# Optimization experiments

Hardware: AMD Instinct MI355X
Metric: run time of the kernel (lower is better)

The kernel has to match this reference:

```python
import jax, jax.numpy as jnp
import numpy as np

N = 50000      # nodes
E = 640000     # edges
D = 128        # emb_dim
IN_DIM = 64    # raw node feature dim
L = 5          # num_layer
BN_EPS = 1e-5


def setup_inputs() -> dict:
    key = jax.random.key(0)
    ks = jax.random.split(key, 12)
    s = 0.05  # modest init scale
    return {
        "x": jax.random.normal(ks[0], (N, IN_DIM), jnp.float32),
        "edge_index": jax.random.randint(ks[1], (2, E), 0, N, jnp.int32),
        "edge_attr": jax.random.normal(ks[2], (E, 13), jnp.float32),
        "atom_W": jax.random.normal(ks[3], (IN_DIM, D), jnp.float32) * s,
        "atom_b": jnp.zeros((D,), jnp.float32),
        "bond_W": jax.random.normal(ks[4], (L, 13, D), jnp.float32) * s,
        "bond_b": jnp.zeros((L, D), jnp.float32),
        "W1": jax.random.normal(ks[5], (L, D, 2 * D), jnp.float32) * s,
        "b1": jnp.zeros((L, 2 * D), jnp.float32),
        "bn1_g": jnp.ones((L, 2 * D), jnp.float32),
        "bn1_b": jnp.zeros((L, 2 * D), jnp.float32),
        "W2": jax.random.normal(ks[6], (L, 2 * D, D), jnp.float32) * s,
        "b2": jnp.zeros((L, D), jnp.float32),
        "eps": jnp.zeros((L,), jnp.float32),
        "bn_g": jnp.ones((L, D), jnp.float32),
        "bn_b": jnp.zeros((L, D), jnp.float32),
    }


def _batchnorm(h, g, b):
    # training-mode BatchNorm1d: batch stats over node axis, biased variance
    mu = jnp.mean(h, axis=0)
    var = jnp.mean(jnp.square(h - mu), axis=0)
    return g * (h - mu) * jax.lax.rsqrt(var + BN_EPS) + b


def reference(x, edge_index, edge_attr, atom_W, atom_b, bond_W, bond_b,
              W1, b1, bn1_g, bn1_b, W2, b2, eps, bn_g, bn_b):
    src, dst = edge_index[0], edge_index[1]
    n = x.shape[0]
    h = x @ atom_W + atom_b  # atom_encoder, [N, D]
    for l in range(L):
        # GINConv: gather -> add edge embedding -> relu -> scatter-add
        edge_emb = edge_attr @ bond_W[l] + bond_b[l]              # [E, D]
        msg = jax.nn.relu(h[src] + edge_emb)                      # [E, D]
        agg = jax.ops.segment_sum(msg, dst, num_segments=n)       # [N, D]
        z = (1.0 + eps[l]) * h + agg
        # mlp: Linear -> BN -> ReLU -> Linear
        z = _batchnorm(z @ W1[l] + b1[l], bn1_g[l], bn1_b[l])
        z = jax.nn.relu(z)
        z = z @ W2[l] + b2[l]
        # outer batchnorm; relu on all but last layer (dropout is eval no-op)
        z = _batchnorm(z, bn_g[l], bn_b[l])
        if l < L - 1:
            z = jax.nn.relu(z)
        h = z  # residual=False, JK='last'
    return h
```

## Files before the change

kernel.cpp:

```cpp
#include <hip/hip_runtime.h>
#include <stdint.h>

#define N_NODES 50000
#define N_EDGES 640000
#define DIM 128
#define IN_DIM 64
#define LAYERS 5
#define BN_EPS 1e-5f
#define NBLK 782

typedef __attribute__((ext_vector_type(8))) short short8;
typedef __attribute__((ext_vector_type(4))) float f32x4;

__device__ __forceinline__ unsigned short f32_to_bf16(float f) {
    uint32_t u = __float_as_uint(f);
    u += 0x7fffu + ((u >> 16) & 1u);
    return (unsigned short)(u >> 16);
}
__device__ __forceinline__ float bf16_to_f32(unsigned short h) {
    return __uint_as_float(((uint32_t)h) << 16);
}

__global__ void wtrans(const float* __restrict__ W, unsigned short* __restrict__ WH,
                       unsigned short* __restrict__ WL, int K, int NN, int total) {
    int idx = blockIdx.x * 256 + threadIdx.x;
    if (idx >= total) return;
    int per = K * NN;
    int l = idx / per;
    int r = idx - l * per;
    int k = r / NN;
    int n = r - k * NN;
    float v = W[idx];
    unsigned short hi = f32_to_bf16(v);
    unsigned short lo = f32_to_bf16(v - bf16_to_f32(hi));
    WH[l * per + n * K + k] = hi;
    WL[l * per + n * K + k] = lo;
}

__global__ __launch_bounds__(256) void atom_enc(const float* __restrict__ x,
                                                const float* __restrict__ W,
                                                const float* __restrict__ b,
                                                float* __restrict__ h) {
    __shared__ float Wl[IN_DIM * DIM];
    __shared__ float bl[DIM];
    for (int i = threadIdx.x; i < IN_DIM * DIM; i += 256) Wl[i] = W[i];
    if (threadIdx.x < DIM) bl[threadIdx.x] = b[threadIdx.x];
    __syncthreads();
    int col = threadIdx.x & 127;
    int rh  = threadIdx.x >> 7;
    int row0 = blockIdx.x * 32;
    for (int rr = 0; rr < 16; ++rr) {
        int row = row0 + rr * 2 + rh;
        if (row >= N_NODES) return;
        float acc = bl[col];
        const float* xr = x + row * IN_DIM;
        #pragma unroll
        for (int k = 0; k < IN_DIM; k += 4) {
            float4 xv = *(const float4*)(xr + k);
            acc += xv.x * Wl[(k + 0) * DIM + col];
            acc += xv.y * Wl[(k + 1) * DIM + col];
            acc += xv.z * Wl[(k + 2) * DIM + col];
            acc += xv.w * Wl[(k + 3) * DIM + col];
        }
        h[row * DIM + col] = acc;
    }
}

__global__ void count_deg(const int* __restrict__ ei, int* __restrict__ deg) {
    int e = blockIdx.x * 256 + threadIdx.x;
    if (e < N_EDGES) atomicAdd(&deg[ei[N_EDGES + e]], 1);
}

__global__ __launch_bounds__(1024) void scan_off(const int* __restrict__ deg,
                                                 int* __restrict__ off,
                                                 int* __restrict__ cursor) {
    __shared__ int wsum[16];
    __shared__ int carry_s;
    int tid = threadIdx.x, w = tid >> 6, lane = tid & 63;
    if (tid == 0) carry_s = 0;
    __syncthreads();
    for (int base = 0; base < N_NODES; base += 1024) {
        int i = base + tid;
        int v = (i < N_NODES) ? deg[i] : 0;
        int x = v;
        #pragma unroll
        for (int d = 1; d < 64; d <<= 1) {
            int t = __shfl_up(x, d);
            if (lane >= d) x += t;
        }
        if (lane == 63) wsum[w] = x;
        __syncthreads();
        if (w == 0) {
            int s_ = (lane < 16) ? wsum[lane] : 0;
            #pragma unroll
            for (int d = 1; d < 16; d <<= 1) {
                int t = __shfl_up(s_, d);
                if (lane >= d) s_ += t;
            }
            if (lane < 16) wsum[lane] = s_;
        }
        __syncthreads();
        int wbase = (w == 0) ? 0 : wsum[w - 1];
        int excl = carry_s + wbase + x - v;
        if (i < N_NODES) { off[i] = excl; cursor[i] = excl; }
        int chunk_total = wsum[15];
        __syncthreads();
        if (tid == 0) carry_s += chunk_total;
        __syncthreads();
    }
    if (threadIdx.x == 0) off[N_NODES] = carry_s;
}

__global__ void fill_csr(const int* __restrict__ ei, int* __restrict__ cursor,
                         int* __restrict__ esrc, int* __restrict__ eidx) {
    int e = blockIdx.x * 256 + threadIdx.x;
    if (e >= N_EDGES) return;
    int dst = ei[N_EDGES + e];
    int pos = atomicAdd(&cursor[dst], 1);
    esrc[pos] = ei[e];
    eidx[pos] = e;
}

__global__ __launch_bounds__(256) void agg_csr(const int* __restrict__ off,
                                               const int* __restrict__ esrc,
                                               const int* __restrict__ eidx,
                                               const float* __restrict__ ea,
                                               const float* __restrict__ bW,
                                               const float* __restrict__ bb,
                                               const float* __restrict__ h,
                                               const float* __restrict__ eps,
                                               int l, float* __restrict__ zf) {
    __shared__ float Wl[13 * DIM];
    __shared__ float bl[DIM];
    for (int i = threadIdx.x; i < 13 * DIM; i += 256) Wl[i] = bW[i];
    if (threadIdx.x < DIM) bl[threadIdx.x] = bb[threadIdx.x];
    __syncthreads();
    int w = threadIdx.x >> 6, lane = threadIdx.x & 63;
    int n = blockIdx.x * 4 + w;
    int c0 = lane * 2;
    float w0[13], w1[13];
    #pragma unroll
    for (int k = 0; k < 13; ++k) { w0[k] = Wl[k * DIM + c0]; w1[k] = Wl[k * DIM + c0 + 1]; }
    float b0 = bl[c0], b1v = bl[c0 + 1];
    int e0 = __builtin_amdgcn_readfirstlane(off[n]);
    int e1 = __builtin_amdgcn_readfirstlane(off[n + 1]);
    int deg = e1 - e0;
    int t = e0 + lane;
    int my_src = (t < e1) ? esrc[t] : 0;
    int my_eid = (t < e1) ? eidx[t] : 0;
    int cnt = deg < 64 ? deg : 64;
    float ax = 0.f, ay = 0.f;

    float a_[13]; float2 hv;
    if (cnt > 0) {
        int s_ = __shfl(my_src, 0), e_ = __shfl(my_eid, 0);
        const float* p = ea + (size_t)e_ * 13;
        #pragma unroll
        for (int k = 0; k < 13; ++k) a_[k] = p[k];
        hv = *(const float2*)(h + (size_t)s_ * DIM + c0);
    }
    for (int i = 0; i < cnt; ++i) {
        float nb[13]; float2 nh;
        if (i + 1 < cnt) {
            int s_ = __shfl(my_src, i + 1), e_ = __shfl(my_eid, i + 1);
            const float* p = ea + (size_t)e_ * 13;
            #pragma unroll
            for (int k = 0; k < 13; ++k) nb[k] = p[k];
            nh = *(const float2*)(h + (size_t)s_ * DIM + c0);
        }
        float ex = b0, ey = b1v;
        #pragma unroll
        for (int k = 0; k < 13; ++k) {
            ex = fmaf(a_[k], w0[k], ex);
            ey = fmaf(a_[k], w1[k], ey);
        }
        ax += fmaxf(hv.x + ex, 0.f);
        ay += fmaxf(hv.y + ey, 0.f);
        if (i + 1 < cnt) {
            #pragma unroll
            for (int k = 0; k < 13; ++k) a_[k] = nb[k];
            hv = nh;
        }
    }
    for (int s2 = e0 + 64; s2 < e1; ++s2) {
        int src = __builtin_amdgcn_readfirstlane(esrc[s2]);
        int eid = __builtin_amdgcn_readfirstlane(eidx[s2]);
        const float* p = ea + (size_t)eid * 13;
        float ex = b0, ey = b1v;
        #pragma unroll
        for (int k = 0; k < 13; ++k) {
            float a = p[k];
            ex = fmaf(a, w0[k], ex);
            ey = fmaf(a, w1[k], ey);
        }
        float2 hvv = *(const float2*)(h + (size_t)src * DIM + c0);
        ax += fmaxf(hvv.x + ex, 0.f);
        ay += fmaxf(hvv.y + ey, 0.f);
    }
    float sc = 1.0f + eps[l];
    float2 hn = *(const float2*)(h + (size_t)n * DIM + c0);
    float2 o;
    o.x = fmaf(sc, hn.x, ax);
    o.y = fmaf(sc, hn.y, ay);
    *(float2*)(zf + (size_t)n * DIM + c0) = o;
}

template<int K, int NN, int NC, bool FUSE_BN>
__global__ __launch_bounds__(256) void gemm_split(const float* __restrict__ A,
                                                  const unsigned short* __restrict__ BH,
                                                  const unsigned short* __restrict__ BL,
                                                  const float* __restrict__ bias,
                                                  const float* __restrict__ bn_a,
                                                  const float* __restrict__ bn_b,
                                                  float* __restrict__ C,
                                                  float* __restrict__ Ps,
                                                  float* __restrict__ Pss) {
    constexpr int NFRAG = NC / 16;
    __shared__ float red[4][2][NC];
    int w = threadIdx.x >> 6, lane = threadIdx.x & 63;
    int rt = blockIdx.x * 4 + w;
    int row0 = rt * 16;
    int gy = blockIdx.y;
    bool active = row0 < N_NODES;
    int lrow = lane & 15;
    int lk   = (lane >> 4) * 8;
    f32x4 acc[NFRAG];
    #pragma unroll
    for (int f = 0; f < NFRAG; ++f) acc[f] = (f32x4){0.f, 0.f, 0.f, 0.f};
    if (active) {
        const float* Ap = A + (size_t)(row0 + lrow) * K + lk;
        #pragma unroll
        for (int ks = 0; ks < K / 32; ++ks) {
            float av[8];
            *(float4*)(av)     = *(const float4*)(Ap + ks * 32);
            *(float4*)(av + 4) = *(const float4*)(Ap + ks * 32 + 4);
            if (FUSE_BN) {
                #pragma unroll
                for (int j = 0; j < 8; ++j) {
                    int k = ks * 32 + lk + j;
                    av[j] = fmaxf(fmaf(bn_a[k], av[j], bn_b[k]), 0.f);
                }
            }
            short8 ah, al;
            #pragma unroll
            for (int j = 0; j < 8; ++j) {
                unsigned short hi = f32_to_bf16(av[j]);
                ah[j] = (short)hi;
                al[j] = (short)f32_to_bf16(av[j] - bf16_to_f32(hi));
            }
            #pragma unroll
            for (int f = 0; f < NFRAG; ++f) {
                int gcol = gy * NC + f * 16 + lrow;
                short8 bh  = *(const short8*)(BH + (size_t)gcol * K + ks * 32 + lk);
                short8 blv = *(const short8*)(BL + (size_t)gcol * K + ks * 32 + lk);
                acc[f] = __builtin_amdgcn_mfma_f32_16x16x32_bf16(ah, bh,  acc[f], 0, 0, 0);
                acc[f] = __builtin_amdgcn_mfma_f32_16x16x32_bf16(al, bh,  acc[f], 0, 0, 0);
                acc[f] = __builtin_amdgcn_mfma_f32_16x16x32_bf16(ah, blv, acc[f], 0, 0, 0);
            }
        }
    }
    int rbase = row0 + (lane >> 4) * 4;
    #pragma unroll
    for (int f = 0; f < NFRAG; ++f) {
        float cs = 0.f, css = 0.f;
        if (active) {
            int gcol = gy * NC + f * 16 + lrow;
            float bv = bias[gcol];
            #pragma unroll
            for (int r = 0; r < 4; ++r) {
                float v = acc[f][r] + bv;
                C[(size_t)(rbase + r) * NN + gcol] = v;
                cs += v;
                css += v * v;
            }
            cs += __shfl_xor(cs, 16);  css += __shfl_xor(css, 16);
            cs += __shfl_xor(cs, 32);  css += __shfl_xor(css, 32);
        }
        if (lane < 16) {
            red[w][0][f * 16 + lrow] = cs;
            red[w][1][f * 16 + lrow] = css;
        }
    }
    __syncthreads();
    int tid = threadIdx.x;
    if (tid < NC) {
        float v = red[0][0][tid] + red[1][0][tid] + red[2][0][tid] + red[3][0][tid];
        Ps[((size_t)gy * NBLK + blockIdx.x) * NC + tid] = v;
    } else if (tid < 2 * NC) {
        int c = tid - NC;
        float v = red[0][1][c] + red[1][1][c] + red[2][1][c] + red[3][1][c];
        Pss[((size_t)gy * NBLK + blockIdx.x) * NC + c] = v;
    }
}

__global__ void reduce_bn(const float* __restrict__ Ps, const float* __restrict__ Pss,
                          const float* __restrict__ g, const float* __restrict__ bvec,
                          float* __restrict__ a, float* __restrict__ bias,
                          int NC, int C) {
    int w = threadIdx.x >> 6, lane = threadIdx.x & 63;
    int col = blockIdx.x * 4 + w;
    if (col >= C) return;
    int gy = col / NC, lc = col - gy * NC;
    const float* ps  = Ps  + ((size_t)gy * NBLK) * NC + lc;
    const float* pss = Pss + ((size_t)gy * NBLK) * NC + lc;
    float s = 0.f, ss = 0.f;
    for (int b = lane; b < NBLK; b += 64) {
        s  += ps[(size_t)b * NC];
        ss += pss[(size_t)b * NC];
    }
    #pragma unroll
    for (int d = 1; d < 64; d <<= 1) {
        s += __shfl_xor(s, d);
        ss += __shfl_xor(ss, d);
    }
    if (lane == 0) {
        float mu  = s * (1.0f / N_NODES);
        float var = ss * (1.0f / N_NODES) - mu * mu;
        float inv = rsqrtf(var + BN_EPS);
        float av = g[col] * inv;
        a[col] = av;
        bias[col] = bvec[col] - mu * av;
    }
}

__global__ void bn_apply(const float* __restrict__ z, const float* __restrict__ a,
                         const float* __restrict__ bias, float* __restrict__ o,
                         int total, int nmask, int relu) {
    int i = blockIdx.x * 256 + threadIdx.x;
    int base = i * 4;
    if (base >= total) return;
    int col = base & nmask;
    float4 v = *(const float4*)(z + base);
    float4 r;
    r.x = a[col + 0] * v.x + bias[col + 0];
    r.y = a[col + 1] * v.y + bias[col + 1];
    r.z = a[col + 2] * v.z + bias[col + 2];
    r.w = a[col + 3] * v.w + bias[col + 3];
    if (relu) {
        r.x = fmaxf(r.x, 0.f); r.y = fmaxf(r.y, 0.f);
        r.z = fmaxf(r.z, 0.f); r.w = fmaxf(r.w, 0.f);
    }
    *(float4*)(o + base) = r;
}

extern "C" void kernel_launch(void* const* d_in, const int* in_sizes, int n_in,
                              void* d_out, int out_size, void* d_ws, size_t ws_size,
                              hipStream_t stream) {
    const float* x      = (const float*)d_in[0];
    const int*   ei     = (const int*)d_in[1];
    const float* ea     = (const float*)d_in[2];
    const float* atom_W = (const float*)d_in[3];
    const float* atom_b = (const float*)d_in[4];
    const float* bond_W = (const float*)d_in[5];
    const float* bond_b = (const float*)d_in[6];
    const float* W1     = (const float*)d_in[7];
    const float* b1     = (const float*)d_in[8];
    const float* bn1_g  = (const float*)d_in[9];
    const float* bn1_b  = (const float*)d_in[10];
    const float* W2     = (const float*)d_in[11];
    const float* b2     = (const float*)d_in[12];
    const float* eps    = (const float*)d_in[13];
    const float* bn_g   = (const float*)d_in[14];
    const float* bn_b   = (const float*)d_in[15];
    float* out = (float*)d_out;

    uint8_t* ws = (uint8_t*)d_ws;
    float* h   = (float*)(ws + 0);
    float* zf  = (float*)(ws + 25600000);
    float* y1  = (float*)(ws + 51200000);
    unsigned short* W1H = (unsigned short*)(ws + 102400000);
    unsigned short* W1L = (unsigned short*)(ws + 102727680);
    unsigned short* W2H = (unsigned short*)(ws + 103055360);
    unsigned short* W2L = (unsigned short*)(ws + 103383040);
    float* coef  = (float*)(ws + 103710720);
    int* off     = (int*)(ws + 103714816);
    int* cursor  = (int*)(ws + 103914880);
    int* esrc    = (int*)(ws + 104114944);
    int* eidx    = (int*)(ws + 106674944);
    int* deg     = (int*)(ws + 109234944);
    float* Ps1   = (float*)(ws + 109434944);
    float* Pss1  = (float*)(ws + 110235712);
    float* Ps2   = (float*)(ws + 111036480);
    float* Pss2  = (float*)(ws + 111436864);
    float* a1  = coef;       float* bb1 = a1 + 256;
    float* a2  = bb1 + 256;  float* bb2 = a2 + 128;
    float* z2  = zf;

    wtrans<<<640, 256, 0, stream>>>(W1, W1H, W1L, 128, 256, LAYERS * 128 * 256);
    wtrans<<<640, 256, 0, stream>>>(W2, W2H, W2L, 256, 128, LAYERS * 256 * 128);

    atom_enc<<<1563, 256, 0, stream>>>(x, atom_W, atom_b, h);

    hipMemsetAsync(deg, 0, 200000, stream);
    count_deg<<<2500, 256, 0, stream>>>(ei, deg);
    scan_off<<<1, 1024, 0, stream>>>(deg, off, cursor);
    fill_csr<<<2500, 256, 0, stream>>>(ei, cursor, esrc, eidx);

    for (int l = 0; l < LAYERS; ++l) {
        agg_csr<<<12500, 256, 0, stream>>>(
            off, esrc, eidx, ea, bond_W + l * 13 * DIM, bond_b + l * DIM, h, eps, l, zf);

        gemm_split<128, 256, 64, false><<<dim3(NBLK, 4), 256, 0, stream>>>(
            zf, W1H + l * 256 * 128, W1L + l * 256 * 128, b1 + l * 256,
            nullptr, nullptr, y1, Ps1, Pss1);

        reduce_bn<<<64, 256, 0, stream>>>(Ps1, Pss1, bn1_g + l * 256, bn1_b + l * 256,
                                          a1, bb1, 64, 256);

        gemm_split<256, 128, 64, true><<<dim3(NBLK, 2), 256, 0, stream>>>(
            y1, W2H + l * 128 * 256, W2L + l * 128 * 256, b2 + l * 128,
            a1, bb1, z2, Ps2, Pss2);

        reduce_bn<<<32, 256, 0, stream>>>(Ps2, Pss2, bn_g + l * 128, bn_b + l * 128,
                                          a2, bb2, 64, 128);

        bn_apply<<<6250, 256, 0, stream>>>(
            z2, a2, bb2, (l < LAYERS - 1) ? h : out, N_NODES * DIM, 127, (l < LAYERS - 1) ? 1 : 0);
    }
    (void)in_sizes; (void)n_in; (void)out_size; (void)ws_size;
}
```

Baseline: 1.654 ms.

## Store GEMM operands pre-split as bf16 hi/lo and widen column tiles

The aggregation kernel now writes its output already split into bf16 high and low halves, and the first GEMM emits split bf16 output instead of fp32. A new bn_split kernel applies the inner BatchNorm and ReLU in place on the split buffers, so the second GEMM reads ready-made bf16 fragments. This replaces the per-tile conversion and fused BN that were redone for every column block. The column tile widens from 64 to 128, which halves the grid's y dimension and the number of A re-reads, and 64-bit index math becomes 32-bit. The cost is an extra elementwise pass over the 256-wide intermediate and more accumulator registers per wave.

```diff
diff --git a/kernel.cpp b/kernel.cpp
--- a/kernel.cpp
+++ b/kernel.cpp
@@ -129,7 +129,9 @@
                                                const float* __restrict__ bb,
                                                const float* __restrict__ h,
                                                const float* __restrict__ eps,
-                                               int l, float* __restrict__ zf) {
+                                               int l,
+                                               unsigned short* __restrict__ zh,
+                                               unsigned short* __restrict__ zl) {
     __shared__ float Wl[13 * DIM];
     __shared__ float bl[DIM];
     for (int i = threadIdx.x; i < 13 * DIM; i += 256) Wl[i] = bW[i];
@@ -153,20 +155,22 @@
 
     float a_[13]; float2 hv;
     if (cnt > 0) {
-        int s_ = __shfl(my_src, 0), e_ = __shfl(my_eid, 0);
-        const float* p = ea + (size_t)e_ * 13;
+        int s_ = __builtin_amdgcn_readlane(my_src, 0);
+        int e_ = __builtin_amdgcn_readlane(my_eid, 0);
+        const float* p = ea + e_ * 13;
         #pragma unroll
         for (int k = 0; k < 13; ++k) a_[k] = p[k];
-        hv = *(const float2*)(h + (size_t)s_ * DIM + c0);
+        hv = *(const float2*)(h + s_ * DIM + c0);
     }
     for (int i = 0; i < cnt; ++i) {
         float nb[13]; float2 nh;
         if (i + 1 < cnt) {
-            int s_ = __shfl(my_src, i + 1), e_ = __shfl(my_eid, i + 1);
-            const float* p = ea + (size_t)e_ * 13;
+            int s_ = __builtin_amdgcn_readlane(my_src, i + 1);
+            int e_ = __builtin_amdgcn_readlane(my_eid, i + 1);
+            const float* p = ea + e_ * 13;
             #pragma unroll
             for (int k = 0; k < 13; ++k) nb[k] = p[k];
-            nh = *(const float2*)(h + (size_t)s_ * DIM + c0);
+            nh = *(const float2*)(h + s_ * DIM + c0);
         }
         float ex = b0, ey = b1v;
         #pragma unroll
@@ -185,7 +189,7 @@
     for (int s2 = e0 + 64; s2 < e1; ++s2) {
         int src = __builtin_amdgcn_readfirstlane(esrc[s2]);
         int eid = __builtin_amdgcn_readfirstlane(eidx[s2]);
-        const float* p = ea + (size_t)eid * 13;
+        const float* p = ea + eid * 13;
         float ex = b0, ey = b1v;
         #pragma unroll
         for (int k = 0; k < 13; ++k) {
@@ -193,26 +197,32 @@
             ex = fmaf(a, w0[k], ex);
             ey = fmaf(a, w1[k], ey);
         }
-        float2 hvv = *(const float2*)(h + (size_t)src * DIM + c0);
+        float2 hvv = *(const float2*)(h + src * DIM + c0);
         ax += fmaxf(hvv.x + ex, 0.f);
         ay += fmaxf(hvv.y + ey, 0.f);
     }
     float sc = 1.0f + eps[l];
-    float2 hn = *(const float2*)(h + (size_t)n * DIM + c0);
-    float2 o;
-    o.x = fmaf(sc, hn.x, ax);
-    o.y = fmaf(sc, hn.y, ay);
-    *(float2*)(zf + (size_t)n * DIM + c0) = o;
-}
-
-template<int K, int NN, int NC, bool FUSE_BN>
-__global__ __launch_bounds__(256) void gemm_split(const float* __restrict__ A,
+    float2 hn = *(const float2*)(h + n * DIM + c0);
+    float zx = fmaf(sc, hn.x, ax);
+    float zy = fmaf(sc, hn.y, ay);
+    unsigned short hx = f32_to_bf16(zx), hy = f32_to_bf16(zy);
+    ushort2 hiv, lov;
+    hiv.x = hx; hiv.y = hy;
+    lov.x = f32_to_bf16(zx - bf16_to_f32(hx));
+    lov.y = f32_to_bf16(zy - bf16_to_f32(hy));
+    *(ushort2*)(zh + n * DIM + c0) = hiv;
+    *(ushort2*)(zl + n * DIM + c0) = lov;
+}
+
+template<int K, int NN, int NC, bool OSPLIT>
+__global__ __launch_bounds__(256) void gemm_split(const unsigned short* __restrict__ AH,
+                                                  const unsigned short* __restrict__ AL,
                                                   const unsigned short* __restrict__ BH,
                                                   const unsigned short* __restrict__ BL,
                                                   const float* __restrict__ bias,
-                                                  const float* __restrict__ bn_a,
-                                                  const float* __restrict__ bn_b,
-                                                  float* __restrict__ C,
+                                                  float* __restrict__ Cf,
+                                                  unsigned short* __restrict__ CH,
+                                                  unsigned short* __restrict__ CL,
                                                   float* __restrict__ Ps,
                                                   float* __restrict__ Pss) {
     constexpr int NFRAG = NC / 16;
@@ -228,31 +238,16 @@
     #pragma unroll
     for (int f = 0; f < NFRAG; ++f) acc[f] = (f32x4){0.f, 0.f, 0.f, 0.f};
     if (active) {
-        const float* Ap = A + (size_t)(row0 + lrow) * K + lk;
+        int abase = (row0 + lrow) * K + lk;
         #pragma unroll
         for (int ks = 0; ks < K / 32; ++ks) {
-            float av[8];
-            *(float4*)(av)     = *(const float4*)(Ap + ks * 32);
-            *(float4*)(av + 4) = *(const float4*)(Ap + ks * 32 + 4);
-            if (FUSE_BN) {
-                #pragma unroll
-                for (int j = 0; j < 8; ++j) {
-                    int k = ks * 32 + lk + j;
-                    av[j] = fmaxf(fmaf(bn_a[k], av[j], bn_b[k]), 0.f);
-                }
-            }
-            short8 ah, al;
-            #pragma unroll
-            for (int j = 0; j < 8; ++j) {
-                unsigned short hi = f32_to_bf16(av[j]);
-                ah[j] = (short)hi;
-                al[j] = (short)f32_to_bf16(av[j] - bf16_to_f32(hi));
-            }
+            short8 ah = *(const short8*)(AH + abase + ks * 32);
+            short8 al = *(const short8*)(AL + abase + ks * 32);
             #pragma unroll
             for (int f = 0; f < NFRAG; ++f) {
                 int gcol = gy * NC + f * 16 + lrow;
-                short8 bh  = *(const short8*)(BH + (size_t)gcol * K + ks * 32 + lk);
-                short8 blv = *(const short8*)(BL + (size_t)gcol * K + ks * 32 + lk);
+                short8 bh  = *(const short8*)(BH + gcol * K + ks * 32 + lk);
+                short8 blv = *(const short8*)(BL + gcol * K + ks * 32 + lk);
                 acc[f] = __builtin_amdgcn_mfma_f32_16x16x32_bf16(ah, bh,  acc[f], 0, 0, 0);
                 acc[f] = __builtin_amdgcn_mfma_f32_16x16x32_bf16(al, bh,  acc[f], 0, 0, 0);
                 acc[f] = __builtin_amdgcn_mfma_f32_16x16x32_bf16(ah, blv, acc[f], 0, 0, 0);
@@ -269,7 +264,14 @@
             #pragma unroll
             for (int r = 0; r < 4; ++r) {
                 float v = acc[f][r] + bv;
-                C[(size_t)(rbase + r) * NN + gcol] = v;
+                int idx = (rbase + r) * NN + gcol;
+                if (OSPLIT) {
+                    unsigned short hi = f32_to_bf16(v);
+                    CH[idx] = hi;
+                    CL[idx] = f32_to_bf16(v - bf16_to_f32(hi));
+                } else {
+                    Cf[idx] = v;
+                }
                 cs += v;
                 css += v * v;
             }
@@ -285,11 +287,11 @@
     int tid = threadIdx.x;
     if (tid < NC) {
         float v = red[0][0][tid] + red[1][0][tid] + red[2][0][tid] + red[3][0][tid];
-        Ps[((size_t)gy * NBLK + blockIdx.x) * NC + tid] = v;
+        Ps[(gy * NBLK + blockIdx.x) * NC + tid] = v;
     } else if (tid < 2 * NC) {
         int c = tid - NC;
         float v = red[0][1][c] + red[1][1][c] + red[2][1][c] + red[3][1][c];
-        Pss[((size_t)gy * NBLK + blockIdx.x) * NC + c] = v;
+        Pss[(gy * NBLK + blockIdx.x) * NC + c] = v;
     }
 }
 
@@ -301,12 +303,12 @@
     int col = blockIdx.x * 4 + w;
     if (col >= C) return;
     int gy = col / NC, lc = col - gy * NC;
-    const float* ps  = Ps  + ((size_t)gy * NBLK) * NC + lc;
-    const float* pss = Pss + ((size_t)gy * NBLK) * NC + lc;
+    const float* ps  = Ps  + (gy * NBLK) * NC + lc;
+    const float* pss = Pss + (gy * NBLK) * NC + lc;
     float s = 0.f, ss = 0.f;
     for (int b = lane; b < NBLK; b += 64) {
-        s  += ps[(size_t)b * NC];
-        ss += pss[(size_t)b * NC];
+        s  += ps[b * NC];
+        ss += pss[b * NC];
     }
     #pragma unroll
     for (int d = 1; d < 64; d <<= 1) {
@@ -321,6 +323,32 @@
         a[col] = av;
         bias[col] = bvec[col] - mu * av;
     }
+}
+
+__global__ void bn_split(unsigned short* __restrict__ yh, unsigned short* __restrict__ yl,
+                         const float* __restrict__ a, const float* __restrict__ bias,
+                         int total, int nmask) {
+    int i = blockIdx.x * 256 + threadIdx.x;
+    int base = i * 4;
+    if (base >= total) return;
+    int col = base & nmask;
+    ushort4 hv = *(const ushort4*)(yh + base);
+    ushort4 lv = *(const ushort4*)(yl + base);
+    float v[4] = {
+        bf16_to_f32(hv.x) + bf16_to_f32(lv.x),
+        bf16_to_f32(hv.y) + bf16_to_f32(lv.y),
+        bf16_to_f32(hv.z) + bf16_to_f32(lv.z),
+        bf16_to_f32(hv.w) + bf16_to_f32(lv.w),
+    };
+    unsigned short ho[4], lo[4];
+    #pragma unroll
+    for (int j = 0; j < 4; ++j) {
+        float r = fmaxf(fmaf(a[col + j], v[j], bias[col + j]), 0.f);
+        ho[j] = f32_to_bf16(r);
+        lo[j] = f32_to_bf16(r - bf16_to_f32(ho[j]));
+    }
+    *(ushort4*)(yh + base) = make_ushort4(ho[0], ho[1], ho[2], ho[3]);
+    *(ushort4*)(yl + base) = make_ushort4(lo[0], lo[1], lo[2], lo[3]);
 }
 
 __global__ void bn_apply(const float* __restrict__ z, const float* __restrict__ a,
@@ -365,9 +393,12 @@
     float* out = (float*)d_out;
 
     uint8_t* ws = (uint8_t*)d_ws;
-    float* h   = (float*)(ws + 0);
-    float* zf  = (float*)(ws + 25600000);
-    float* y1  = (float*)(ws + 51200000);
+    float* h            = (float*)(ws + 0);
+    unsigned short* zh  = (unsigned short*)(ws + 25600000);
+    unsigned short* zl  = (unsigned short*)(ws + 38400000);
+    float* z2           = (float*)(ws + 25600000);
+    unsigned short* y1h = (unsigned short*)(ws + 51200000);
+    unsigned short* y1l = (unsigned short*)(ws + 76800000);
     unsigned short* W1H = (unsigned short*)(ws + 102400000);
     unsigned short* W1L = (unsigned short*)(ws + 102727680);
     unsigned short* W2H = (unsigned short*)(ws + 103055360);
@@ -384,7 +415,6 @@
     float* Pss2  = (float*)(ws + 111436864);
     float* a1  = coef;       float* bb1 = a1 + 256;
     float* a2  = bb1 + 256;  float* bb2 = a2 + 128;
-    float* z2  = zf;
 
     wtrans<<<640, 256, 0, stream>>>(W1, W1H, W1L, 128, 256, LAYERS * 128 * 256);
     wtrans<<<640, 256, 0, stream>>>(W2, W2H, W2L, 256, 128, LAYERS * 256 * 128);
@@ -398,21 +428,23 @@
 
     for (int l = 0; l < LAYERS; ++l) {
         agg_csr<<<12500, 256, 0, stream>>>(
-            off, esrc, eidx, ea, bond_W + l * 13 * DIM, bond_b + l * DIM, h, eps, l, zf);
-
-        gemm_split<128, 256, 64, false><<<dim3(NBLK, 4), 256, 0, stream>>>(
-            zf, W1H + l * 256 * 128, W1L + l * 256 * 128, b1 + l * 256,
-            nullptr, nullptr, y1, Ps1, Pss1);
+            off, esrc, eidx, ea, bond_W + l * 13 * DIM, bond_b + l * DIM, h, eps, l, zh, zl);
+
+        gemm_split<128, 256, 128, true><<<dim3(NBLK, 2), 256, 0, stream>>>(
+            zh, zl, W1H + l * 256 * 128, W1L + l * 256 * 128, b1 + l * 256,
+            nullptr, y1h, y1l, Ps1, Pss1);
 
         reduce_bn<<<64, 256, 0, stream>>>(Ps1, Pss1, bn1_g + l * 256, bn1_b + l * 256,
-                                          a1, bb1, 64, 256);
-
-        gemm_split<256, 128, 64, true><<<dim3(NBLK, 2), 256, 0, stream>>>(
-            y1, W2H + l * 128 * 256, W2L + l * 128 * 256, b2 + l * 128,
-            a1, bb1, z2, Ps2, Pss2);
+                                          a1, bb1, 128, 256);
+
+        bn_split<<<12500, 256, 0, stream>>>(y1h, y1l, a1, bb1, N_NODES * 256, 255);
+
+        gemm_split<256, 128, 128, false><<<dim3(NBLK, 1), 256, 0, stream>>>(
+            y1h, y1l, W2H + l * 128 * 256, W2L + l * 128 * 256, b2 + l * 128,
+            z2, nullptr, nullptr, Ps2, Pss2);
 
         reduce_bn<<<32, 256, 0, stream>>>(Ps2, Pss2, bn_g + l * 128, bn_b + l * 128,
-                                          a2, bb2, 64, 128);
+                                          a2, bb2, 128, 128);
 
         bn_apply<<<6250, 256, 0, stream>>>(
             z2, a2, bb2, (l < LAYERS - 1) ? h : out, N_NODES * DIM, 127, (l < LAYERS - 1) ? 1 : 0);
```

Measured after the change: 1.612 ms. -2.6%, faster.

## Use bf16 gathers with CSR-sorted edge attrs and pre-split GEMM inputs

Applied to the files above, without the earlier changes.

Edge attributes are permuted into CSR order once and stored as padded bf16, and a bf16 copy of h is kept for the neighbor gathers. The aggregation kernel now emits hi/lo bf16 splits directly, so the first GEMM skips the fp32-to-bf16 conversion. Both GEMMs also now cover all output columns in a single block column instead of several. The aim is to cut gather bandwidth and indirection in the memory-bound aggregation, at the cost of reduced precision in h and the edge features during message computation.

```diff
diff --git a/kernel.cpp b/kernel.cpp
--- a/kernel.cpp
+++ b/kernel.cpp
@@ -40,7 +40,8 @@
 __global__ __launch_bounds__(256) void atom_enc(const float* __restrict__ x,
                                                 const float* __restrict__ W,
                                                 const float* __restrict__ b,
-                                                float* __restrict__ h) {
+                                                float* __restrict__ h,
+                                                unsigned short* __restrict__ hb) {
     __shared__ float Wl[IN_DIM * DIM];
     __shared__ float bl[DIM];
     for (int i = threadIdx.x; i < IN_DIM * DIM; i += 256) Wl[i] = W[i];
@@ -63,6 +64,7 @@
             acc += xv.w * Wl[(k + 3) * DIM + col];
         }
         h[row * DIM + col] = acc;
+        hb[row * DIM + col] = f32_to_bf16(acc);
     }
 }
 
@@ -121,15 +123,29 @@
     eidx[pos] = e;
 }
 
+__global__ void ea_sort(const int* __restrict__ eidx, const float* __restrict__ ea,
+                        unsigned short* __restrict__ eas) {
+    int s = blockIdx.x * 256 + threadIdx.x;
+    if (s >= N_EDGES) return;
+    int e = eidx[s];
+    const float* p = ea + (size_t)e * 13;
+    unsigned short* q = eas + (size_t)s * 14;
+    #pragma unroll
+    for (int k = 0; k < 13; ++k) q[k] = f32_to_bf16(p[k]);
+    q[13] = 0;
+}
+
 __global__ __launch_bounds__(256) void agg_csr(const int* __restrict__ off,
                                                const int* __restrict__ esrc,
-                                               const int* __restrict__ eidx,
-                                               const float* __restrict__ ea,
+                                               const uint32_t* __restrict__ eas32,
                                                const float* __restrict__ bW,
                                                const float* __restrict__ bb,
                                                const float* __restrict__ h,
+                                               const uint32_t* __restrict__ hb32,
                                                const float* __restrict__ eps,
-                                               int l, float* __restrict__ zf) {
+                                               int l,
+                                               unsigned short* __restrict__ zh,
+                                               unsigned short* __restrict__ zl) {
     __shared__ float Wl[13 * DIM];
     __shared__ float bl[DIM];
     for (int i = threadIdx.x; i < 13 * DIM; i += 256) Wl[i] = bW[i];
@@ -147,79 +163,81 @@
     int deg = e1 - e0;
     int t = e0 + lane;
     int my_src = (t < e1) ? esrc[t] : 0;
-    int my_eid = (t < e1) ? eidx[t] : 0;
     int cnt = deg < 64 ? deg : 64;
     float ax = 0.f, ay = 0.f;
 
-    float a_[13]; float2 hv;
-    if (cnt > 0) {
-        int s_ = __shfl(my_src, 0), e_ = __shfl(my_eid, 0);
-        const float* p = ea + (size_t)e_ * 13;
-        #pragma unroll
-        for (int k = 0; k < 13; ++k) a_[k] = p[k];
-        hv = *(const float2*)(h + (size_t)s_ * DIM + c0);
-    }
-    for (int i = 0; i < cnt; ++i) {
-        float nb[13]; float2 nh;
-        if (i + 1 < cnt) {
-            int s_ = __shfl(my_src, i + 1), e_ = __shfl(my_eid, i + 1);
-            const float* p = ea + (size_t)e_ * 13;
-            #pragma unroll
-            for (int k = 0; k < 13; ++k) nb[k] = p[k];
-            nh = *(const float2*)(h + (size_t)s_ * DIM + c0);
-        }
+    uint32_t eA[7], eB[7];
+    uint32_t hA = 0, hB = 0;
+
+    auto LOAD = [&](int i, uint32_t* eD, uint32_t& hD) {
+        int s_ = __builtin_amdgcn_readlane(my_src, i);
+        const uint32_t* p = eas32 + (size_t)(e0 + i) * 7;
+        #pragma unroll
+        for (int k = 0; k < 7; ++k) eD[k] = p[k];
+        hD = hb32[s_ * (DIM / 2) + lane];
+    };
+    auto COMPUTE = [&](const uint32_t* eD, uint32_t hD) {
+        float f[13];
+        #pragma unroll
+        for (int k = 0; k < 6; ++k) {
+            f[2 * k]     = __uint_as_float(eD[k] << 16);
+            f[2 * k + 1] = __uint_as_float(eD[k] & 0xffff0000u);
+        }
+        f[12] = __uint_as_float(eD[6] << 16);
         float ex = b0, ey = b1v;
         #pragma unroll
         for (int k = 0; k < 13; ++k) {
-            ex = fmaf(a_[k], w0[k], ex);
-            ey = fmaf(a_[k], w1[k], ey);
-        }
-        ax += fmaxf(hv.x + ex, 0.f);
-        ay += fmaxf(hv.y + ey, 0.f);
-        if (i + 1 < cnt) {
-            #pragma unroll
-            for (int k = 0; k < 13; ++k) a_[k] = nb[k];
-            hv = nh;
-        }
+            ex = fmaf(f[k], w0[k], ex);
+            ey = fmaf(f[k], w1[k], ey);
+        }
+        float hx = __uint_as_float(hD << 16);
+        float hy = __uint_as_float(hD & 0xffff0000u);
+        ax += fmaxf(hx + ex, 0.f);
+        ay += fmaxf(hy + ey, 0.f);
+    };
+
+    if (cnt > 0) LOAD(0, eA, hA);
+    for (int i = 0; i < cnt; i += 2) {
+        if (i + 1 < cnt) LOAD(i + 1, eB, hB);
+        COMPUTE(eA, hA);
+        if (i + 2 < cnt) LOAD(i + 2, eA, hA);
+        if (i + 1 < cnt) COMPUTE(eB, hB);
     }
     for (int s2 = e0 + 64; s2 < e1; ++s2) {
         int src = __builtin_amdgcn_readfirstlane(esrc[s2]);
-        int eid = __builtin_amdgcn_readfirstlane(eidx[s2]);
-        const float* p = ea + (size_t)eid * 13;
-        float ex = b0, ey = b1v;
-        #pragma unroll
-        for (int k = 0; k < 13; ++k) {
-            float a = p[k];
-            ex = fmaf(a, w0[k], ex);
-            ey = fmaf(a, w1[k], ey);
-        }
-        float2 hvv = *(const float2*)(h + (size_t)src * DIM + c0);
-        ax += fmaxf(hvv.x + ex, 0.f);
-        ay += fmaxf(hvv.y + ey, 0.f);
-    }
+        uint32_t eT[7];
+        const uint32_t* p = eas32 + (size_t)s2 * 7;
+        #pragma unroll
+        for (int k = 0; k < 7; ++k) eT[k] = p[k];
+        COMPUTE(eT, hb32[src * (DIM / 2) + lane]);
+    }
+
     float sc = 1.0f + eps[l];
     float2 hn = *(const float2*)(h + (size_t)n * DIM + c0);
-    float2 o;
-    o.x = fmaf(sc, hn.x, ax);
-    o.y = fmaf(sc, hn.y, ay);
-    *(float2*)(zf + (size_t)n * DIM + c0) = o;
-}
-
-template<int K, int NN, int NC, bool FUSE_BN>
-__global__ __launch_bounds__(256) void gemm_split(const float* __restrict__ A,
-                                                  const unsigned short* __restrict__ BH,
-                                                  const unsigned short* __restrict__ BL,
-                                                  const float* __restrict__ bias,
-                                                  const float* __restrict__ bn_a,
-                                                  const float* __restrict__ bn_b,
-                                                  float* __restrict__ C,
-                                                  float* __restrict__ Ps,
-                                                  float* __restrict__ Pss) {
+    float zx = fmaf(sc, hn.x, ax);
+    float zy = fmaf(sc, hn.y, ay);
+    unsigned short hx = f32_to_bf16(zx), hy = f32_to_bf16(zy);
+    ushort2 hiv, lov;
+    hiv.x = hx; hiv.y = hy;
+    lov.x = f32_to_bf16(zx - bf16_to_f32(hx));
+    lov.y = f32_to_bf16(zy - bf16_to_f32(hy));
+    *(ushort2*)(zh + (size_t)n * DIM + c0) = hiv;
+    *(ushort2*)(zl + (size_t)n * DIM + c0) = lov;
+}
+
+template<int K, int NN, int NC>
+__global__ __launch_bounds__(256) void gemm1_split(const unsigned short* __restrict__ AH,
+                                                   const unsigned short* __restrict__ AL,
+                                                   const unsigned short* __restrict__ BH,
+                                                   const unsigned short* __restrict__ BL,
+                                                   const float* __restrict__ bias,
+                                                   float* __restrict__ Cf,
+                                                   float* __restrict__ Ps,
+                                                   float* __restrict__ Pss) {
     constexpr int NFRAG = NC / 16;
     __shared__ float red[4][2][NC];
     int w = threadIdx.x >> 6, lane = threadIdx.x & 63;
-    int rt = blockIdx.x * 4 + w;
-    int row0 = rt * 16;
+    int row0 = (blockIdx.x * 4 + w) * 16;
     int gy = blockIdx.y;
     bool active = row0 < N_NODES;
     int lrow = lane & 15;
@@ -228,25 +246,98 @@
     #pragma unroll
     for (int f = 0; f < NFRAG; ++f) acc[f] = (f32x4){0.f, 0.f, 0.f, 0.f};
     if (active) {
+        int abase = (row0 + lrow) * K + lk;
+        #pragma unroll
+        for (int ks = 0; ks < K / 32; ++ks) {
+            short8 ah = *(const short8*)(AH + abase + ks * 32);
+            short8 al = *(const short8*)(AL + abase + ks * 32);
+            #pragma unroll
+            for (int f = 0; f < NFRAG; ++f) {
+                int gcol = gy * NC + f * 16 + lrow;
+                short8 bh  = *(const short8*)(BH + (size_t)gcol * K + ks * 32 + lk);
+                short8 blv = *(const short8*)(BL + (size_t)gcol * K + ks * 32 + lk);
+                acc[f] = __builtin_amdgcn_mfma_f32_16x16x32_bf16(ah, bh,  acc[f], 0, 0, 0);
+                acc[f] = __builtin_amdgcn_mfma_f32_16x16x32_bf16(al, bh,  acc[f], 0, 0, 0);
+                acc[f] = __builtin_amdgcn_mfma_f32_16x16x32_bf16(ah, blv, acc[f], 0, 0, 0);
+            }
+        }
+    }
+    int rbase = row0 + (lane >> 4) * 4;
+    #pragma unroll
+    for (int f = 0; f < NFRAG; ++f) {
+        float cs = 0.f, css = 0.f;
+        if (active) {
+            int gcol = gy * NC + f * 16 + lrow;
+            float bv = bias[gcol];
+            #pragma unroll
+            for (int r = 0; r < 4; ++r) {
+                float v = acc[f][r] + bv;
+                Cf[(size_t)(rbase + r) * NN + gcol] = v;
+                cs += v;
+                css += v * v;
+            }
+            cs += __shfl_xor(cs, 16);  css += __shfl_xor(css, 16);
+            cs += __shfl_xor(cs, 32);  css += __shfl_xor(css, 32);
+        }
+        if (lane < 16) {
+            red[w][0][f * 16 + lrow] = cs;
+            red[w][1][f * 16 + lrow] = css;
+        }
+    }
+    __syncthreads();
+    int tid = threadIdx.x;
+    for (int c = tid; c < NC; c += 256) {
+        float v = red[0][0][c] + red[1][0][c] + red[2][0][c] + red[3][0][c];
+        Ps[((size_t)gy * NBLK + blockIdx.x) * NC + c] = v;
+    }
+    for (int c = tid; c < NC; c += 256) {
+        float v = red[0][1][c] + red[1][1][c] + red[2][1][c] + red[3][1][c];
+        Pss[((size_t)gy * NBLK + blockIdx.x) * NC + c] = v;
+    }
+}
+
+template<int K, int NN, int NC>
+__global__ __launch_bounds__(256) void gemm_bn(const float* __restrict__ A,
+                                               const unsigned short* __restrict__ BH,
+                                               const unsigned short* __restrict__ BL,
+                                               const float* __restrict__ bias,
+                                               const float* __restrict__ bn_a,
+                                               const float* __restrict__ bn_b,
+                                               float* __restrict__ Cf,
+                                               float* __restrict__ Ps,
+                                               float* __restrict__ Pss) {
+    constexpr int NFRAG = NC / 16;
+    __shared__ float red[4][2][NC];
+    int w = threadIdx.x >> 6, lane = threadIdx.x & 63;
+    int row0 = (blockIdx.x * 4 + w) * 16;
+    int gy = blockIdx.y;
+    bool active = row0 < N_NODES;
+    int lrow = lane & 15;
+    int lk   = (lane >> 4) * 8;
+    f32x4 acc[NFRAG];
+    #pragma unroll
+    for (int f = 0; f < NFRAG; ++f) acc[f] = (f32x4){0.f, 0.f, 0.f, 0.f};
+    if (active) {
         const float* Ap = A + (size_t)(row0 + lrow) * K + lk;
         #pragma unroll
         for (int ks = 0; ks < K / 32; ++ks) {
             float av[8];
             *(float4*)(av)     = *(const float4*)(Ap + ks * 32);
             *(float4*)(av + 4) = *(const float4*)(Ap + ks * 32 + 4);
-            if (FUSE_BN) {
-                #pragma unroll
-                for (int j = 0; j < 8; ++j) {
-                    int k = ks * 32 + lk + j;
-                    av[j] = fmaxf(fmaf(bn_a[k], av[j], bn_b[k]), 0.f);
-                }
-            }
+            int k0 = ks * 32 + lk;
+            float4 ba0 = *(const float4*)(bn_a + k0);
+            float4 ba1 = *(const float4*)(bn_a + k0 + 4);
+            float4 bb0 = *(const float4*)(bn_b + k0);
+            float4 bb1 = *(const float4*)(bn_b + k0 + 4);
+            float aa[8] = {ba0.x, ba0.y, ba0.z, ba0.w, ba1.x, ba1.y, ba1.z, ba1.w};
+            float ab[8] = {bb0.x, bb0.y, bb0.z, bb0.w, bb1.x, bb1.y, bb1.z, bb1.w};
             short8 ah, al;
             #pragma unroll
             for (int j = 0; j < 8; ++j) {
-                unsigned short hi = f32_to_bf16(av[j]);
+                float v = fmaxf(fmaf(aa[j], av[j], ab[j]), 0.f);
+                unsigned short hi = f32_to_bf16(v);
                 ah[j] = (short)hi;
-                al[j] = (short)f32_to_bf16(av[j] - bf16_to_f32(hi));
+                al[j] = (short)f32_to_bf16(v - bf16_to_f32(hi));
             }
             #pragma unroll
             for (int f = 0; f < NFRAG; ++f) {
@@ -269,7 +360,7 @@
             #pragma unroll
             for (int r = 0; r < 4; ++r) {
                 float v = acc[f][r] + bv;
-                C[(size_t)(rbase + r) * NN + gcol] = v;
+                Cf[(size_t)(rbase + r) * NN + gcol] = v;
                 cs += v;
                 css += v * v;
             }
@@ -283,11 +374,11 @@
     }
     __syncthreads();
     int tid = threadIdx.x;
-    if (tid < NC) {
-        float v = red[0][0][tid] + red[1][0][tid] + red[2][0][tid] + red[3][0][tid];
-        Ps[((size_t)gy * NBLK + blockIdx.x) * NC + tid] = v;
-    } else if (tid < 2 * NC) {
-        int c = tid - NC;
+    for (int c = tid; c < NC; c += 256) {
+        float v = red[0][0][c] + red[1][0][c] + red[2][0][c] + red[3][0][c];
+        Ps[((size_t)gy * NBLK + blockIdx.x) * NC + c] = v;
+    }
+    for (int c = tid; c < NC; c += 256) {
         float v = red[0][1][c] + red[1][1][c] + red[2][1][c] + red[3][1][c];
         Pss[((size_t)gy * NBLK + blockIdx.x) * NC + c] = v;
     }
@@ -325,6 +416,7 @@
 
 __global__ void bn_apply(const float* __restrict__ z, const float* __restrict__ a,
                          const float* __restrict__ bias, float* __restrict__ o,
+                         unsigned short* __restrict__ hbout,
                          int total, int nmask, int relu) {
     int i = blockIdx.x * 256 + threadIdx.x;
     int base = i * 4;
@@ -341,6 +433,12 @@
         r.z = fmaxf(r.z, 0.f); r.w = fmaxf(r.w, 0.f);
     }
     *(float4*)(o + base) = r;
+    if (hbout) {
+        ushort4 u;
+        u.x = f32_to_bf16(r.x); u.y = f32_to_bf16(r.y);
+        u.z = f32_to_bf16(r.z); u.w = f32_to_bf16(r.w);
+        *(ushort4*)(hbout + base) = u;
+    }
 }
 
 extern "C" void kernel_launch(void* const* d_in, const int* in_sizes, int n_in,
@@ -365,57 +463,64 @@
     float* out = (float*)d_out;
 
     uint8_t* ws = (uint8_t*)d_ws;
-    float* h   = (float*)(ws + 0);
-    float* zf  = (float*)(ws + 25600000);
-    float* y1  = (float*)(ws + 51200000);
-    unsigned short* W1H = (unsigned short*)(ws + 102400000);
-    unsigned short* W1L = (unsigned short*)(ws + 102727680);
-    unsigned short* W2H = (unsigned short*)(ws + 103055360);
-    unsigned short* W2L = (unsigned short*)(ws + 103383040);
-    float* coef  = (float*)(ws + 103710720);
-    int* off     = (int*)(ws + 103714816);
-    int* cursor  = (int*)(ws + 103914880);
-    int* esrc    = (int*)(ws + 104114944);
-    int* eidx    = (int*)(ws + 106674944);
-    int* deg     = (int*)(ws + 109234944);
-    float* Ps1   = (float*)(ws + 109434944);
-    float* Pss1  = (float*)(ws + 110235712);
-    float* Ps2   = (float*)(ws + 111036480);
-    float* Pss2  = (float*)(ws + 111436864);
+    float* h            = (float*)(ws + 0);
+    unsigned short* hb  = (unsigned short*)(ws + 25600000);
+    unsigned short* zh  = (unsigned short*)(ws + 38400000);
+    unsigned short* zl  = (unsigned short*)(ws + 51200000);
+    float* z2           = (float*)(ws + 38400000);
+    float* y1           = (float*)(ws + 64000000);
+    unsigned short* eas = (unsigned short*)(ws + 115200000);
+    unsigned short* W1H = (unsigned short*)(ws + 133120000);
+    unsigned short* W1L = (unsigned short*)(ws + 133447680);
+    unsigned short* W2H = (unsigned short*)(ws + 133775360);
+    unsigned short* W2L = (unsigned short*)(ws + 134103040);
+    float* coef  = (float*)(ws + 134430720);
+    int* off     = (int*)(ws + 134434816);
+    int* esrc    = (int*)(ws + 134634880);
+    float* Ps1   = (float*)(ws + 137194880);
+    float* Pss1  = (float*)(ws + 137995648);
+    float* Ps2   = (float*)(ws + 138796416);
+    float* Pss2  = (float*)(ws + 139196800);
+    int* cursor  = (int*)(ws + 64000000);
+    int* eidx    = (int*)(ws + 64200064);
+    int* deg     = (int*)(ws + 66760064);
     float* a1  = coef;       float* bb1 = a1 + 256;
     float* a2  = bb1 + 256;  float* bb2 = a2 + 128;
-    float* z2  = zf;
 
     wtrans<<<640, 256, 0, stream>>>(W1, W1H, W1L, 128, 256, LAYERS * 128 * 256);
     wtrans<<<640, 256, 0, stream>>>(W2, W2H, W2L, 256, 128, LAYERS * 256 * 128);
 
-    atom_enc<<<1563, 256, 0, stream>>>(x, atom_W, atom_b, h);
+    atom_enc<<<1563, 256, 0, stream>>>(x, atom_W, atom_b, h, hb);
 
     hipMemsetAsync(deg, 0, 200000, stream);
     count_deg<<<2500, 256, 0, stream>>>(ei, deg);
     scan_off<<<1, 1024, 0, stream>>>(deg, off, cursor);
     fill_csr<<<2500, 256, 0, stream>>>(ei, cursor, esrc, eidx);
+    ea_sort<<<2500, 256, 0, stream>>>(eidx, ea, eas);
 
     for (int l = 0; l < LAYERS; ++l) {
         agg_csr<<<12500, 256, 0, stream>>>(
-            off, esrc, eidx, ea, bond_W + l * 13 * DIM, bond_b + l * DIM, h, eps, l, zf);
-
-        gemm_split<128, 256, 64, false><<<dim3(NBLK, 4), 256, 0, stream>>>(
-            zf, W1H + l * 256 * 128, W1L + l * 256 * 128, b1 + l * 256,
-            nullptr, nullptr, y1, Ps1, Pss1);
+            off, esrc, (const uint32_t*)eas, bond_W + l * 13 * DIM, bond_b + l * DIM,
+            h, (const uint32_t*)hb, eps, l, zh, zl);
+
+        gemm1_split<128, 256, 256><<<dim3(NBLK, 1), 256, 0, stream>>>(
+            zh, zl, W1H + l * 256 * 128, W1L + l * 256 * 128, b1 + l * 256,
+            y1, Ps1, Pss1);
 
         reduce_bn<<<64, 256, 0, stream>>>(Ps1, Pss1, bn1_g + l * 256, bn1_b + l * 256,
-                                          a1, bb1, 64, 256);
-
-        gemm_split<256, 128, 64, true><<<dim3(NBLK, 2), 256, 0, stream>>>(
+                                          a1, bb1, 256, 256);
+
+        gemm_bn<256, 128, 128><<<dim3(NBLK, 1), 256, 0, stream>>>(
             y1, W2H + l * 128 * 256, W2L + l * 128 * 256, b2 + l * 128,
             a1, bb1, z2, Ps2, Pss2);
 
         reduce_bn<<<32, 256, 0, stream>>>(Ps2, Pss2, bn_g + l * 128, bn_b + l * 128,
-                                          a2, bb2, 64, 128);
-
+                                          a2, bb2, 128, 128);
+
+        int last = (l == LAYERS - 1);
         bn_apply<<<6250, 256, 0, stream>>>(
-            z2, a2, bb2, (l < LAYERS - 1) ? h : out, N_NODES * DIM, 127, (l < LAYERS - 1) ? 1 : 0);
+            z2, a2, bb2, last ? out : h, last ? (unsigned short*)nullptr : hb,
+            N_NODES * DIM, 127, last ? 0 : 1);
     }
     (void)in_sizes; (void)n_in; (void)out_size; (void)ws_size;
 }
```

Result: faster. 1.585 ms (-4.2%).
